# Optimization experiments

Hardware: AMD Instinct MI355X
Metric: run time of the kernel (lower is better)

Reference implementation:

```python
import jax, jax.numpy as jnp
import numpy as np


def _dct2(x):
    """DCT-II over last dim, scipy norm=None scaling (matches the torch rfft trick:
    X_k = 2 * sum_n x_n cos(pi*k*(2n+1)/(2N))). Expressed as one batched matmul."""
    N = x.shape[-1]
    n = jnp.arange(N, dtype=x.dtype)
    k = jnp.arange(N, dtype=x.dtype)
    # D[k, n] = 2*cos(pi*k*(2n+1)/(2N))
    D = 2.0 * jnp.cos((np.pi / (2.0 * N)) * k[:, None] * (2.0 * n[None, :] + 1.0))
    return jnp.einsum('kn,bcn->bck', D, x)


def setup_inputs() -> dict:
    key = jax.random.key(0)
    k0, k1, k2 = jax.random.split(key, 3)
    b, c, l = 32, 512, 1024
    x = jax.random.normal(k0, (b, c, l), dtype=jnp.float32)
    # 1x1 Conv1d weights (kernel_size=1, bias=False) stored as [out, in]
    w1 = jax.random.normal(k1, (2 * c, c), dtype=jnp.float32) / np.float32(np.sqrt(c))
    w2 = jax.random.normal(k2, (c, 2 * c), dtype=jnp.float32) / np.float32(np.sqrt(2 * c))
    ln_w = jnp.ones((l,), dtype=jnp.float32)
    ln_b = jnp.zeros((l,), dtype=jnp.float32)
    return {"x": x, "w1": w1, "w2": w2, "ln_w": ln_w, "ln_b": ln_b}


def reference(x, w1, w2, ln_w, ln_b):
    eps = 1e-6
    freq = _dct2(x)                                   # [b, c, l]
    mu = jnp.mean(freq, axis=-1, keepdims=True)
    var = jnp.var(freq, axis=-1, keepdims=True)       # biased, like nn.LayerNorm
    h = (freq - mu) * jax.lax.rsqrt(var + eps) * ln_w + ln_b
    # fc: Conv1d(c->2c, k=1) -> Dropout(eval: identity) -> ReLU -> Conv1d(2c->c) -> Sigmoid
    h = jax.nn.relu(jnp.einsum('oi,bil->bol', w1, h))  # [b, 2c, l]
    gate = jax.nn.sigmoid(jnp.einsum('oi,bil->bol', w2, h))  # [b, c, l]
    return x * gate
```

## Files before the change

### kernel.cpp

```cpp
#include <hip/hip_runtime.h>
#include <hip/hip_bf16.h>
#include <math.h>

typedef short short8 __attribute__((ext_vector_type(8)));
typedef short short4v __attribute__((ext_vector_type(4)));
typedef float f32x4 __attribute__((ext_vector_type(4)));

__device__ __forceinline__ short f2bf(float f) {
  union { float f; unsigned u; } v; v.f = f;
  unsigned r = v.u + 0x7FFFu + ((v.u >> 16) & 1u);
  return (short)(r >> 16);
}
__device__ __forceinline__ float bf2f(short s) {
  union { unsigned u; float f; } v; v.u = ((unsigned)(unsigned short)s) << 16;
  return v.f;
}

__global__ __launch_bounds__(256) void cast_kernel(const float* __restrict__ in,
                                                   short* __restrict__ out, int n4) {
  int i = blockIdx.x * blockDim.x + threadIdx.x;
  if (i < n4) {
    float4 v = ((const float4*)in)[i];
    short4v o;
    o.x = f2bf(v.x); o.y = f2bf(v.y); o.z = f2bf(v.z); o.w = f2bf(v.w);
    ((short4v*)out)[i] = o;
  }
}

__global__ __launch_bounds__(256) void build_D(short* __restrict__ D) {
  int t = blockIdx.x * 256 + threadIdx.x;
  int k = t >> 10, n = t & 1023;
  const float s = 1.5339807878856412e-03f;
  float arg = (s * (float)k) * (float)(2 * n + 1);
  D[t] = f2bf(2.0f * cosf(arg));
}

__global__ __launch_bounds__(256) void ln_stats(const float2* __restrict__ partial,
                                                float2* __restrict__ musd) {
  int n = blockIdx.x * 256 + threadIdx.x;
  float S = 0.f, Q = 0.f;
#pragma unroll
  for (int r = 0; r < 4; ++r) {
    float2 p = partial[(size_t)r * 16384 + n];
    S += p.x; Q += p.y;
  }
  float mu  = S * (1.f / 1024.f);
  float var = Q * (1.f / 1024.f) - mu * mu;
  float2 o; o.x = mu; o.y = rsqrtf(var + 1e-6f);
  musd[n] = o;
}

__global__ __launch_bounds__(256) void ln_apply(short* __restrict__ freqT,
                                                const float2* __restrict__ musd,
                                                const float* __restrict__ lnw,
                                                const float* __restrict__ lnb) {
  int t = blockIdx.x * 256 + threadIdx.x;
  int c8 = t & 63;
  int k  = (t >> 6) & 1023;
  int b  = t >> 16;
  size_t idx = ((size_t)b << 19) + (size_t)k * 512 + (size_t)c8 * 8;
  short8 v = *(const short8*)&freqT[idx];
  float w  = lnw[k];
  float bb = lnb[k];
  const float2* ms = &musd[b * 512 + c8 * 8];
  short8 o;
#pragma unroll
  for (int j = 0; j < 8; ++j) {
    float f = bf2f(v[j]);
    float2 m = ms[j];
    o[j] = f2bf((f - m.x) * m.y * w + bb);
  }
  *(short8*)&freqT[idx] = o;
}

template<int EPI>
__global__ __launch_bounds__(512, 2) void gemm256(
    const short* __restrict__ A, const short* __restrict__ B,
    void* __restrict__ Cout, const float* __restrict__ X,
    float2* __restrict__ P, int K, int NT, long strideA, long strideB)
{
  __shared__ short As[2][16384];
  __shared__ short Bs[2][16384];
  const int tid = threadIdx.x;
  const int l   = tid & 63;
  const int w   = tid >> 6;
  const int wm  = w >> 2;
  const int wn  = w & 3;
  const int l7  = l & 7;
  const int lr  = l & 15;
  const int lhi = l >> 4;

  const int nwg = gridDim.x, q = nwg >> 3, orig = blockIdx.x;
  const int wgid = (orig & 7) * q + (orig >> 3);
  int bx, by, bz;
  if (EPI == 0)      { bx = wgid & 3; by = wgid >> 2;      bz = 0; }
  else if (EPI == 1) { bx = wgid & 3; by = (wgid >> 2) & 3; bz = wgid >> 4; }
  else               { by = wgid & 3; bx = (wgid >> 2) & 1; bz = wgid >> 3; }

  const long row0 = (long)bx * 256, col0 = (long)by * 256;
  const short* Ab = A + (size_t)bz * strideA + (size_t)row0 * K;
  const short* Bb = B + (size_t)bz * strideB + (size_t)col0 * K;

  const int rowb  = w * 8 + (l >> 3);
  const int colel = (l7 ^ (l >> 3)) * 8;
  const int arow = (wm * 128 + lr) * 64;
  const int brow = (wn * 64  + lr) * 64;
  const int sk0 = ((lhi    ) ^ l7) * 8;
  const int sk1 = ((lhi + 4) ^ l7) * 8;

  f32x4 acc[8][4];
#pragma unroll
  for (int i = 0; i < 8; ++i)
#pragma unroll
    for (int j = 0; j < 4; ++j) acc[i][j] = (f32x4){0.f, 0.f, 0.f, 0.f};

#define STAGE(KT, D) do {                                                    \
    const size_t ko_ = (size_t)(KT) * 64 + colel;                            \
    _Pragma("unroll")                                                        \
    for (int r_ = 0; r_ < 4; ++r_)                                           \
      __builtin_amdgcn_global_load_lds(                                      \
        (const __attribute__((address_space(1))) void*)(Ab + (size_t)(r_*64 + rowb)*K + ko_), \
        (__attribute__((address_space(3))) void*)(&As[D][r_*4096 + w*512 + l*8]), 16, 0, 0);  \
    _Pragma("unroll")                                                        \
    for (int r_ = 0; r_ < 4; ++r_)                                           \
      __builtin_amdgcn_global_load_lds(                                      \
        (const __attribute__((address_space(1))) void*)(Bb + (size_t)(r_*64 + rowb)*K + ko_), \
        (__attribute__((address_space(3))) void*)(&Bs[D][r_*4096 + w*512 + l*8]), 16, 0, 0);  \
  } while (0)

  STAGE(0, 0);
  STAGE(1, 1);

  short8 b0, b1, b2, b3;
  int cur = 0;
  for (int kt = 0; kt < NT; ++kt) {
    if (kt + 1 < NT) { asm volatile("s_waitcnt vmcnt(8)" ::: "memory"); }
    else             { asm volatile("s_waitcnt vmcnt(0)" ::: "memory"); }
    __builtin_amdgcn_sched_barrier(0);
    __builtin_amdgcn_s_barrier();
    const short* Ad = As[cur];
    const short* Bd = Bs[cur];
    short8 a0, a1, a2, a3;

#define MFMA_ROW(MI, AV)                                                       \
    acc[MI][0] = __builtin_amdgcn_mfma_f32_16x16x32_bf16(AV, b0, acc[MI][0], 0, 0, 0); \
    acc[MI][1] = __builtin_amdgcn_mfma_f32_16x16x32_bf16(AV, b1, acc[MI][1], 0, 0, 0); \
    acc[MI][2] = __builtin_amdgcn_mfma_f32_16x16x32_bf16(AV, b2, acc[MI][2], 0, 0, 0); \
    acc[MI][3] = __builtin_amdgcn_mfma_f32_16x16x32_bf16(AV, b3, acc[MI][3], 0, 0, 0);

#define PH(MIBASE, SK, LOADB)                                                \
    a0 = *(const short8*)&Ad[arow + (MIBASE + 0) * 1024 + SK];               \
    a1 = *(const short8*)&Ad[arow + (MIBASE + 1) * 1024 + SK];               \
    a2 = *(const short8*)&Ad[arow + (MIBASE + 2) * 1024 + SK];               \
    a3 = *(const short8*)&Ad[arow + (MIBASE + 3) * 1024 + SK];               \
    if (LOADB) {                                                             \
      b0 = *(const short8*)&Bd[brow + 0 * 1024 + SK];                        \
      b1 = *(const short8*)&Bd[brow + 1 * 1024 + SK];                        \
      b2 = *(const short8*)&Bd[brow + 2 * 1024 + SK];                        \
      b3 = *(const short8*)&Bd[brow + 3 * 1024 + SK];                        \
    }                                                                        \
    __builtin_amdgcn_s_barrier();                                            \
    asm volatile("s_waitcnt lgkmcnt(0)" ::: "memory");                       \
    __builtin_amdgcn_sched_barrier(0);                                       \
    __builtin_amdgcn_s_setprio(1);                                           \
    MFMA_ROW(MIBASE + 0, a0); MFMA_ROW(MIBASE + 1, a1);                      \
    MFMA_ROW(MIBASE + 2, a2); MFMA_ROW(MIBASE + 3, a3);                      \
    __builtin_amdgcn_s_setprio(0);                                           \
    __builtin_amdgcn_sched_barrier(0);                                       \
    __builtin_amdgcn_s_barrier();

    PH(0, sk0, 1)
    PH(4, sk0, 0)
    PH(0, sk1, 1)
    PH(4, sk1, 0)

    if (kt + 2 < NT) STAGE(kt + 2, cur);
    cur ^= 1;
  }

  const int rb = (int)row0 + wm * 128 + lhi * 4;
  const int cb = (int)col0 + wn * 64 + lr;
  float sv[4], qv[4];
#pragma unroll
  for (int ni = 0; ni < 4; ++ni) { sv[ni] = 0.f; qv[ni] = 0.f; }

#pragma unroll
  for (int mi = 0; mi < 8; ++mi) {
#pragma unroll
    for (int ni = 0; ni < 4; ++ni) {
#pragma unroll
      for (int j = 0; j < 4; ++j) {
        int r  = rb + mi * 16 + j;
        int cc = cb + ni * 16;
        float v = acc[mi][ni][j];
        if (EPI == 0) {
          sv[ni] += v; qv[ni] += v * v;
          ((short*)Cout)[((size_t)(cc >> 9) << 19) + (size_t)r * 512 + (cc & 511)] = f2bf(v);
        } else if (EPI == 1) {
          ((short*)Cout)[(size_t)bz * 1048576 + (size_t)r * 1024 + cc] = f2bf(v > 0.f ? v : 0.f);
        } else {
          size_t idx = (size_t)bz * 524288 + (size_t)r * 1024 + cc;
          float g = 1.f / (1.f + __expf(-v));
          ((float*)Cout)[idx] = X[idx] * g;
        }
      }
    }
  }

  if (EPI == 0) {
    __syncthreads();
    float* redS = (float*)&As[0][0];
    float* redQ = redS + 2048;
    const int contrib = wm * 4 + lhi;
#pragma unroll
    for (int ni = 0; ni < 4; ++ni) {
      int ccl = wn * 64 + ni * 16 + lr;
      redS[ccl * 8 + contrib] = sv[ni];
      redQ[ccl * 8 + contrib] = qv[ni];
    }
    __syncthreads();
    if (tid < 256) {
      float S = 0.f, Q = 0.f;
#pragma unroll
      for (int i = 0; i < 8; ++i) { S += redS[tid * 8 + i]; Q += redQ[tid * 8 + i]; }
      float2 o; o.x = S; o.y = Q;
      P[(size_t)bx * 16384 + col0 + tid] = o;
    }
  }
#undef PH
#undef MFMA_ROW
#undef STAGE
}

extern "C" void kernel_launch(void* const* d_in, const int* in_sizes, int n_in,
                              void* d_out, int out_size, void* d_ws, size_t ws_size,
                              hipStream_t stream) {
  const float* x    = (const float*)d_in[0];
  const float* w1   = (const float*)d_in[1];
  const float* w2   = (const float*)d_in[2];
  const float* ln_w = (const float*)d_in[3];
  const float* ln_b = (const float*)d_in[4];
  float* out = (float*)d_out;

  char* ws = (char*)d_ws;
  short* x_bf   = (short*)(ws);
  short* D_bf   = (short*)(ws + 33554432);
  short* w1_bf  = (short*)(ws + 35651584);
  short* w2_bf  = (short*)(ws + 36700160);
  short* freqT  = (short*)(ws + 37748736);
  short* z1t    = (short*)(ws + 71303168);
  float2* part  = (float2*)(ws + 138412032);
  float2* musd  = (float2*)(ws + 139460608);

  cast_kernel<<<dim3(16384), dim3(256), 0, stream>>>(x,  x_bf,  16777216 / 4);
  cast_kernel<<<dim3(512),   dim3(256), 0, stream>>>(w1, w1_bf, 524288 / 4);
  cast_kernel<<<dim3(512),   dim3(256), 0, stream>>>(w2, w2_bf, 524288 / 4);
  build_D<<<dim3(4096), dim3(256), 0, stream>>>(D_bf);

  gemm256<0><<<dim3(256), dim3(512), 0, stream>>>(
      D_bf, x_bf, (void*)freqT, nullptr, part, 1024, 16, 0, 0);

  ln_stats<<<dim3(64), dim3(256), 0, stream>>>(part, musd);

  ln_apply<<<dim3(8192), dim3(256), 0, stream>>>(freqT, musd, ln_w, ln_b);

  gemm256<1><<<dim3(512), dim3(512), 0, stream>>>(
      freqT, w1_bf, (void*)z1t, nullptr, nullptr, 512, 8, 524288, 0);

  gemm256<2><<<dim3(256), dim3(512), 0, stream>>>(
      w2_bf, z1t, (void*)out, x, nullptr, 1024, 16, 0, 1048576);
}
```

Baseline: 193.0 us.

## Halve GEMM N-tile, deepen B pipeline, read bf16 x in gate epilogue

New measurement: 212.7 us. +10.2%, slower.

```diff
diff --git a/kernel.cpp b/kernel.cpp
--- a/kernel.cpp
+++ b/kernel.cpp
@@ -76,11 +76,11 @@
 template<int EPI>
 __global__ __launch_bounds__(512, 2) void gemm256(
     const short* __restrict__ A, const short* __restrict__ B,
-    void* __restrict__ Cout, const float* __restrict__ X,
+    void* __restrict__ Cout, const short* __restrict__ XB,
     float2* __restrict__ P, int K, int NT, long strideA, long strideB)
 {
   __shared__ short As[2][16384];
-  __shared__ short Bs[2][16384];
+  __shared__ short Bs[4][8192];
   const int tid = threadIdx.x;
   const int l   = tid & 63;
   const int w   = tid >> 6;
@@ -93,101 +93,109 @@
   const int nwg = gridDim.x, q = nwg >> 3, orig = blockIdx.x;
   const int wgid = (orig & 7) * q + (orig >> 3);
   int bx, by, bz;
-  if (EPI == 0)      { bx = wgid & 3; by = wgid >> 2;      bz = 0; }
-  else if (EPI == 1) { bx = wgid & 3; by = (wgid >> 2) & 3; bz = wgid >> 4; }
-  else               { by = wgid & 3; bx = (wgid >> 2) & 1; bz = wgid >> 3; }
-
-  const long row0 = (long)bx * 256, col0 = (long)by * 256;
+  if (EPI == 0)      { bx = wgid & 3; by = wgid >> 2;       bz = 0; }
+  else if (EPI == 1) { bx = wgid & 3; by = (wgid >> 2) & 7; bz = wgid >> 5; }
+  else               { bx = wgid & 1; by = (wgid >> 1) & 7; bz = wgid >> 4; }
+
+  const long row0 = (long)bx * 256, col0 = (long)by * 128;
   const short* Ab = A + (size_t)bz * strideA + (size_t)row0 * K;
   const short* Bb = B + (size_t)bz * strideB + (size_t)col0 * K;
 
   const int rowb  = w * 8 + (l >> 3);
   const int colel = (l7 ^ (l >> 3)) * 8;
-  const int arow = (wm * 128 + lr) * 64;
-  const int brow = (wn * 64  + lr) * 64;
+  const int arow  = (wm * 128 + lr) * 64;
+  const int brow0 = (wn * 32 + lr) * 64;
+  const int brow1 = brow0 + 1024;
   const int sk0 = ((lhi    ) ^ l7) * 8;
   const int sk1 = ((lhi + 4) ^ l7) * 8;
 
-  f32x4 acc[8][4];
-#pragma unroll
-  for (int i = 0; i < 8; ++i)
-#pragma unroll
-    for (int j = 0; j < 4; ++j) acc[i][j] = (f32x4){0.f, 0.f, 0.f, 0.f};
-
-#define STAGE(KT, D) do {                                                    \
+  f32x4 acc[8][2];
+#pragma unroll
+  for (int i = 0; i < 8; ++i) { acc[i][0] = (f32x4){0,0,0,0}; acc[i][1] = (f32x4){0,0,0,0}; }
+
+#define GLL(SRC, DST) __builtin_amdgcn_global_load_lds(                      \
+      (const __attribute__((address_space(1))) void*)(SRC),                  \
+      (__attribute__((address_space(3))) void*)(DST), 16, 0, 0)
+
+#define STAGE_A(KT, D) do {                                                  \
     const size_t ko_ = (size_t)(KT) * 64 + colel;                            \
     _Pragma("unroll")                                                        \
     for (int r_ = 0; r_ < 4; ++r_)                                           \
-      __builtin_amdgcn_global_load_lds(                                      \
-        (const __attribute__((address_space(1))) void*)(Ab + (size_t)(r_*64 + rowb)*K + ko_), \
-        (__attribute__((address_space(3))) void*)(&As[D][r_*4096 + w*512 + l*8]), 16, 0, 0);  \
-    _Pragma("unroll")                                                        \
-    for (int r_ = 0; r_ < 4; ++r_)                                           \
-      __builtin_amdgcn_global_load_lds(                                      \
-        (const __attribute__((address_space(1))) void*)(Bb + (size_t)(r_*64 + rowb)*K + ko_), \
-        (__attribute__((address_space(3))) void*)(&Bs[D][r_*4096 + w*512 + l*8]), 16, 0, 0);  \
+      GLL(Ab + (size_t)(r_ * 64 + rowb) * K + ko_,                           \
+          &As[D][r_ * 4096 + w * 512 + l * 8]);                              \
   } while (0)
 
-  STAGE(0, 0);
-  STAGE(1, 1);
-
-  short8 b0, b1, b2, b3;
-  int cur = 0;
-  for (int kt = 0; kt < NT; ++kt) {
-    if (kt + 1 < NT) { asm volatile("s_waitcnt vmcnt(8)" ::: "memory"); }
-    else             { asm volatile("s_waitcnt vmcnt(0)" ::: "memory"); }
-    __builtin_amdgcn_sched_barrier(0);
-    __builtin_amdgcn_s_barrier();
-    const short* Ad = As[cur];
-    const short* Bd = Bs[cur];
-    short8 a0, a1, a2, a3;
-
-#define MFMA_ROW(MI, AV)                                                       \
-    acc[MI][0] = __builtin_amdgcn_mfma_f32_16x16x32_bf16(AV, b0, acc[MI][0], 0, 0, 0); \
-    acc[MI][1] = __builtin_amdgcn_mfma_f32_16x16x32_bf16(AV, b1, acc[MI][1], 0, 0, 0); \
-    acc[MI][2] = __builtin_amdgcn_mfma_f32_16x16x32_bf16(AV, b2, acc[MI][2], 0, 0, 0); \
-    acc[MI][3] = __builtin_amdgcn_mfma_f32_16x16x32_bf16(AV, b3, acc[MI][3], 0, 0, 0);
-
-#define PH(MIBASE, SK, LOADB)                                                \
-    a0 = *(const short8*)&Ad[arow + (MIBASE + 0) * 1024 + SK];               \
-    a1 = *(const short8*)&Ad[arow + (MIBASE + 1) * 1024 + SK];               \
-    a2 = *(const short8*)&Ad[arow + (MIBASE + 2) * 1024 + SK];               \
-    a3 = *(const short8*)&Ad[arow + (MIBASE + 3) * 1024 + SK];               \
-    if (LOADB) {                                                             \
-      b0 = *(const short8*)&Bd[brow + 0 * 1024 + SK];                        \
-      b1 = *(const short8*)&Bd[brow + 1 * 1024 + SK];                        \
-      b2 = *(const short8*)&Bd[brow + 2 * 1024 + SK];                        \
-      b3 = *(const short8*)&Bd[brow + 3 * 1024 + SK];                        \
-    }                                                                        \
+#define STAGE_B_Q(KT, S, R) do {                                             \
+    const size_t ko_ = (size_t)(KT) * 64 + colel;                            \
+    GLL(Bb + (size_t)((R) * 64 + rowb) * K + ko_,                            \
+        &Bs[S][(R) * 4096 + w * 512 + l * 8]);                               \
+  } while (0)
+
+  STAGE_B_Q(0, 0, 0); STAGE_B_Q(0, 0, 1);
+  STAGE_B_Q(1, 1, 0); STAGE_B_Q(1, 1, 1);
+  STAGE_A(0, 0);
+  STAGE_B_Q(2, 2, 0); STAGE_B_Q(2, 2, 1);
+  STAGE_A(1, 1);
+
+#define MFMA(AV, BV, C) __builtin_amdgcn_mfma_f32_16x16x32_bf16(AV, BV, C, 0, 0, 0)
+
+#define PH2(SK, SR)                                                          \
+    a0 = *(const short8*)&Ad[arow + 0 * 1024 + (SK)];                        \
+    a1 = *(const short8*)&Ad[arow + 1 * 1024 + (SK)];                        \
+    a2 = *(const short8*)&Ad[arow + 2 * 1024 + (SK)];                        \
+    a3 = *(const short8*)&Ad[arow + 3 * 1024 + (SK)];                        \
+    a4 = *(const short8*)&Ad[arow + 4 * 1024 + (SK)];                        \
+    a5 = *(const short8*)&Ad[arow + 5 * 1024 + (SK)];                        \
+    a6 = *(const short8*)&Ad[arow + 6 * 1024 + (SK)];                        \
+    a7 = *(const short8*)&Ad[arow + 7 * 1024 + (SK)];                        \
+    b0 = *(const short8*)&Bd[brow0 + (SK)];                                  \
+    b1 = *(const short8*)&Bd[brow1 + (SK)];                                  \
+    if (doB) STAGE_B_Q(kt + 3, sB, SR);                                      \
     __builtin_amdgcn_s_barrier();                                            \
     asm volatile("s_waitcnt lgkmcnt(0)" ::: "memory");                       \
     __builtin_amdgcn_sched_barrier(0);                                       \
     __builtin_amdgcn_s_setprio(1);                                           \
-    MFMA_ROW(MIBASE + 0, a0); MFMA_ROW(MIBASE + 1, a1);                      \
-    MFMA_ROW(MIBASE + 2, a2); MFMA_ROW(MIBASE + 3, a3);                      \
+    acc[0][0] = MFMA(a0, b0, acc[0][0]); acc[0][1] = MFMA(a0, b1, acc[0][1]); \
+    acc[1][0] = MFMA(a1, b0, acc[1][0]); acc[1][1] = MFMA(a1, b1, acc[1][1]); \
+    acc[2][0] = MFMA(a2, b0, acc[2][0]); acc[2][1] = MFMA(a2, b1, acc[2][1]); \
+    acc[3][0] = MFMA(a3, b0, acc[3][0]); acc[3][1] = MFMA(a3, b1, acc[3][1]); \
+    acc[4][0] = MFMA(a4, b0, acc[4][0]); acc[4][1] = MFMA(a4, b1, acc[4][1]); \
+    acc[5][0] = MFMA(a5, b0, acc[5][0]); acc[5][1] = MFMA(a5, b1, acc[5][1]); \
+    acc[6][0] = MFMA(a6, b0, acc[6][0]); acc[6][1] = MFMA(a6, b1, acc[6][1]); \
+    acc[7][0] = MFMA(a7, b0, acc[7][0]); acc[7][1] = MFMA(a7, b1, acc[7][1]); \
     __builtin_amdgcn_s_setprio(0);                                           \
     __builtin_amdgcn_sched_barrier(0);                                       \
     __builtin_amdgcn_s_barrier();
 
-    PH(0, sk0, 1)
-    PH(4, sk0, 0)
-    PH(0, sk1, 1)
-    PH(4, sk1, 0)
-
-    if (kt + 2 < NT) STAGE(kt + 2, cur);
+  int cur = 0;
+  for (int kt = 0; kt < NT; ++kt) {
+    if (kt + 2 < NT)       { asm volatile("s_waitcnt vmcnt(6)" ::: "memory"); }
+    else if (kt + 2 == NT) { asm volatile("s_waitcnt vmcnt(4)" ::: "memory"); }
+    else                   { asm volatile("s_waitcnt vmcnt(0)" ::: "memory"); }
+    __builtin_amdgcn_sched_barrier(0);
+    __builtin_amdgcn_s_barrier();
+    const short* Ad = As[cur];
+    const short* Bd = Bs[kt & 3];
+    const int sB = (kt + 3) & 3;
+    const bool doB = (kt + 3) < NT;
+    short8 a0, a1, a2, a3, a4, a5, a6, a7, b0, b1;
+
+    PH2(sk0, 0)
+    PH2(sk1, 1)
+
+    if (kt + 2 < NT) STAGE_A(kt + 2, cur);
     cur ^= 1;
   }
 
   const int rb = (int)row0 + wm * 128 + lhi * 4;
-  const int cb = (int)col0 + wn * 64 + lr;
-  float sv[4], qv[4];
-#pragma unroll
-  for (int ni = 0; ni < 4; ++ni) { sv[ni] = 0.f; qv[ni] = 0.f; }
+  const int cb = (int)col0 + wn * 32 + lr;
+  float sv[2], qv[2];
+  sv[0] = sv[1] = qv[0] = qv[1] = 0.f;
 
 #pragma unroll
   for (int mi = 0; mi < 8; ++mi) {
 #pragma unroll
-    for (int ni = 0; ni < 4; ++ni) {
+    for (int ni = 0; ni < 2; ++ni) {
 #pragma unroll
       for (int j = 0; j < 4; ++j) {
         int r  = rb + mi * 16 + j;
@@ -201,7 +209,7 @@
         } else {
           size_t idx = (size_t)bz * 524288 + (size_t)r * 1024 + cc;
           float g = 1.f / (1.f + __expf(-v));
-          ((float*)Cout)[idx] = X[idx] * g;
+          ((float*)Cout)[idx] = bf2f(XB[idx]) * g;
         }
       }
     }
@@ -210,16 +218,16 @@
   if (EPI == 0) {
     __syncthreads();
     float* redS = (float*)&As[0][0];
-    float* redQ = redS + 2048;
+    float* redQ = redS + 1024;
     const int contrib = wm * 4 + lhi;
 #pragma unroll
-    for (int ni = 0; ni < 4; ++ni) {
-      int ccl = wn * 64 + ni * 16 + lr;
+    for (int ni = 0; ni < 2; ++ni) {
+      int ccl = wn * 32 + ni * 16 + lr;
       redS[ccl * 8 + contrib] = sv[ni];
       redQ[ccl * 8 + contrib] = qv[ni];
     }
     __syncthreads();
-    if (tid < 256) {
+    if (tid < 128) {
       float S = 0.f, Q = 0.f;
 #pragma unroll
       for (int i = 0; i < 8; ++i) { S += redS[tid * 8 + i]; Q += redQ[tid * 8 + i]; }
@@ -227,9 +235,11 @@
       P[(size_t)bx * 16384 + col0 + tid] = o;
     }
   }
-#undef PH
-#undef MFMA_ROW
-#undef STAGE
+#undef PH2
+#undef MFMA
+#undef STAGE_A
+#undef STAGE_B_Q
+#undef GLL
 }
 
 extern "C" void kernel_launch(void* const* d_in, const int* in_sizes, int n_in,
@@ -257,16 +267,16 @@
   cast_kernel<<<dim3(512),   dim3(256), 0, stream>>>(w2, w2_bf, 524288 / 4);
   build_D<<<dim3(4096), dim3(256), 0, stream>>>(D_bf);
 
-  gemm256<0><<<dim3(256), dim3(512), 0, stream>>>(
+  gemm256<0><<<dim3(512), dim3(512), 0, stream>>>(
       D_bf, x_bf, (void*)freqT, nullptr, part, 1024, 16, 0, 0);
 
   ln_stats<<<dim3(64), dim3(256), 0, stream>>>(part, musd);
 
   ln_apply<<<dim3(8192), dim3(256), 0, stream>>>(freqT, musd, ln_w, ln_b);
 
-  gemm256<1><<<dim3(512), dim3(512), 0, stream>>>(
+  gemm256<1><<<dim3(1024), dim3(512), 0, stream>>>(
       freqT, w1_bf, (void*)z1t, nullptr, nullptr, 512, 8, 524288, 0);
 
-  gemm256<2><<<dim3(256), dim3(512), 0, stream>>>(
-      w2_bf, z1t, (void*)out, x, nullptr, 1024, 16, 0, 1048576);
-}
+  gemm256<2><<<dim3(512), dim3(512), 0, stream>>>(
+      w2_bf, z1t, (void*)out, x_bf, nullptr, 1024, 16, 0, 1048576);
+}
```

## Restructure GEMM main loop for LDS-load/MFMA overlap and read bf16 x in epilogue

Applied to the files above, without the earlier changes.

Result: faster. 166.5 us (-13.7%).

```diff
diff --git a/kernel.cpp b/kernel.cpp
--- a/kernel.cpp
+++ b/kernel.cpp
@@ -76,7 +76,7 @@
 template<int EPI>
 __global__ __launch_bounds__(512, 2) void gemm256(
     const short* __restrict__ A, const short* __restrict__ B,
-    void* __restrict__ Cout, const float* __restrict__ X,
+    void* __restrict__ Cout, const short* __restrict__ XB,
     float2* __restrict__ P, int K, int NT, long strideA, long strideB)
 {
   __shared__ short As[2][16384];
@@ -93,7 +93,7 @@
   const int nwg = gridDim.x, q = nwg >> 3, orig = blockIdx.x;
   const int wgid = (orig & 7) * q + (orig >> 3);
   int bx, by, bz;
-  if (EPI == 0)      { bx = wgid & 3; by = wgid >> 2;      bz = 0; }
+  if (EPI == 0)      { bx = wgid & 3; by = wgid >> 2;       bz = 0; }
   else if (EPI == 1) { bx = wgid & 3; by = (wgid >> 2) & 3; bz = wgid >> 4; }
   else               { by = wgid & 3; bx = (wgid >> 2) & 1; bz = wgid >> 3; }
 
@@ -114,67 +114,106 @@
 #pragma unroll
     for (int j = 0; j < 4; ++j) acc[i][j] = (f32x4){0.f, 0.f, 0.f, 0.f};
 
+#define GLL(SRC, DST) __builtin_amdgcn_global_load_lds(                      \
+      (const __attribute__((address_space(1))) void*)(SRC),                  \
+      (__attribute__((address_space(3))) void*)(DST), 16, 0, 0)
+
 #define STAGE(KT, D) do {                                                    \
     const size_t ko_ = (size_t)(KT) * 64 + colel;                            \
     _Pragma("unroll")                                                        \
     for (int r_ = 0; r_ < 4; ++r_)                                           \
-      __builtin_amdgcn_global_load_lds(                                      \
-        (const __attribute__((address_space(1))) void*)(Ab + (size_t)(r_*64 + rowb)*K + ko_), \
-        (__attribute__((address_space(3))) void*)(&As[D][r_*4096 + w*512 + l*8]), 16, 0, 0);  \
+      GLL(Ab + (size_t)(r_ * 64 + rowb) * K + ko_,                           \
+          &As[D][r_ * 4096 + w * 512 + l * 8]);                              \
     _Pragma("unroll")                                                        \
     for (int r_ = 0; r_ < 4; ++r_)                                           \
-      __builtin_amdgcn_global_load_lds(                                      \
-        (const __attribute__((address_space(1))) void*)(Bb + (size_t)(r_*64 + rowb)*K + ko_), \
-        (__attribute__((address_space(3))) void*)(&Bs[D][r_*4096 + w*512 + l*8]), 16, 0, 0);  \
+      GLL(Bb + (size_t)(r_ * 64 + rowb) * K + ko_,                           \
+          &Bs[D][r_ * 4096 + w * 512 + l * 8]);                              \
   } while (0)
 
   STAGE(0, 0);
   STAGE(1, 1);
 
-  short8 b0, b1, b2, b3;
+#define MFMA(AV, BV, C) __builtin_amdgcn_mfma_f32_16x16x32_bf16(AV, BV, C, 0, 0, 0)
+#define QUAD(M0, V0, V1, V2, V3)                                             \
+    __builtin_amdgcn_s_setprio(1);                                           \
+    acc[M0+0][0] = MFMA(V0, b0, acc[M0+0][0]);                               \
+    acc[M0+0][1] = MFMA(V0, b1, acc[M0+0][1]);                               \
+    acc[M0+0][2] = MFMA(V0, b2, acc[M0+0][2]);                               \
+    acc[M0+0][3] = MFMA(V0, b3, acc[M0+0][3]);                               \
+    acc[M0+1][0] = MFMA(V1, b0, acc[M0+1][0]);                               \
+    acc[M0+1][1] = MFMA(V1, b1, acc[M0+1][1]);                               \
+    acc[M0+1][2] = MFMA(V1, b2, acc[M0+1][2]);                               \
+    acc[M0+1][3] = MFMA(V1, b3, acc[M0+1][3]);                               \
+    acc[M0+2][0] = MFMA(V2, b0, acc[M0+2][0]);                               \
+    acc[M0+2][1] = MFMA(V2, b1, acc[M0+2][1]);                               \
+    acc[M0+2][2] = MFMA(V2, b2, acc[M0+2][2]);                               \
+    acc[M0+2][3] = MFMA(V2, b3, acc[M0+2][3]);                               \
+    acc[M0+3][0] = MFMA(V3, b0, acc[M0+3][0]);                               \
+    acc[M0+3][1] = MFMA(V3, b1, acc[M0+3][1]);                               \
+    acc[M0+3][2] = MFMA(V3, b2, acc[M0+3][2]);                               \
+    acc[M0+3][3] = MFMA(V3, b3, acc[M0+3][3]);                               \
+    __builtin_amdgcn_s_setprio(0);                                           \
+    __builtin_amdgcn_sched_barrier(0);
+
   int cur = 0;
   for (int kt = 0; kt < NT; ++kt) {
-    if (kt + 1 < NT) { asm volatile("s_waitcnt vmcnt(8)" ::: "memory"); }
+    if (kt + 2 < NT) { asm volatile("s_waitcnt vmcnt(8)" ::: "memory"); }
     else             { asm volatile("s_waitcnt vmcnt(0)" ::: "memory"); }
     __builtin_amdgcn_sched_barrier(0);
     __builtin_amdgcn_s_barrier();
     const short* Ad = As[cur];
     const short* Bd = Bs[cur];
-    short8 a0, a1, a2, a3;
-
-#define MFMA_ROW(MI, AV)                                                       \
-    acc[MI][0] = __builtin_amdgcn_mfma_f32_16x16x32_bf16(AV, b0, acc[MI][0], 0, 0, 0); \
-    acc[MI][1] = __builtin_amdgcn_mfma_f32_16x16x32_bf16(AV, b1, acc[MI][1], 0, 0, 0); \
-    acc[MI][2] = __builtin_amdgcn_mfma_f32_16x16x32_bf16(AV, b2, acc[MI][2], 0, 0, 0); \
-    acc[MI][3] = __builtin_amdgcn_mfma_f32_16x16x32_bf16(AV, b3, acc[MI][3], 0, 0, 0);
-
-#define PH(MIBASE, SK, LOADB)                                                \
-    a0 = *(const short8*)&Ad[arow + (MIBASE + 0) * 1024 + SK];               \
-    a1 = *(const short8*)&Ad[arow + (MIBASE + 1) * 1024 + SK];               \
-    a2 = *(const short8*)&Ad[arow + (MIBASE + 2) * 1024 + SK];               \
-    a3 = *(const short8*)&Ad[arow + (MIBASE + 3) * 1024 + SK];               \
-    if (LOADB) {                                                             \
-      b0 = *(const short8*)&Bd[brow + 0 * 1024 + SK];                        \
-      b1 = *(const short8*)&Bd[brow + 1 * 1024 + SK];                        \
-      b2 = *(const short8*)&Bd[brow + 2 * 1024 + SK];                        \
-      b3 = *(const short8*)&Bd[brow + 3 * 1024 + SK];                        \
-    }                                                                        \
-    __builtin_amdgcn_s_barrier();                                            \
-    asm volatile("s_waitcnt lgkmcnt(0)" ::: "memory");                       \
-    __builtin_amdgcn_sched_barrier(0);                                       \
-    __builtin_amdgcn_s_setprio(1);                                           \
-    MFMA_ROW(MIBASE + 0, a0); MFMA_ROW(MIBASE + 1, a1);                      \
-    MFMA_ROW(MIBASE + 2, a2); MFMA_ROW(MIBASE + 3, a3);                      \
-    __builtin_amdgcn_s_setprio(0);                                           \
-    __builtin_amdgcn_sched_barrier(0);                                       \
+    short8 a0, a1, a2, a3, a4, a5, a6, a7;
+    short8 b0, b1, b2, b3;
+
+    a0 = *(const short8*)&Ad[arow + 0 * 1024 + sk0];
+    a1 = *(const short8*)&Ad[arow + 1 * 1024 + sk0];
+    a2 = *(const short8*)&Ad[arow + 2 * 1024 + sk0];
+    a3 = *(const short8*)&Ad[arow + 3 * 1024 + sk0];
+    b0 = *(const short8*)&Bd[brow + 0 * 1024 + sk0];
+    b1 = *(const short8*)&Bd[brow + 1 * 1024 + sk0];
+    b2 = *(const short8*)&Bd[brow + 2 * 1024 + sk0];
+    b3 = *(const short8*)&Bd[brow + 3 * 1024 + sk0];
+    __builtin_amdgcn_sched_barrier(0);
+    a4 = *(const short8*)&Ad[arow + 4 * 1024 + sk0];
+    a5 = *(const short8*)&Ad[arow + 5 * 1024 + sk0];
+    a6 = *(const short8*)&Ad[arow + 6 * 1024 + sk0];
+    a7 = *(const short8*)&Ad[arow + 7 * 1024 + sk0];
+    __builtin_amdgcn_sched_barrier(0);
+    asm volatile("s_waitcnt lgkmcnt(4)" ::: "memory");
+    __builtin_amdgcn_sched_barrier(0);
+    QUAD(0, a0, a1, a2, a3)
+
+    short8 c0, c1, c2, c3, c4, c5, c6, c7, e0, e1, e2, e3;
+    c0 = *(const short8*)&Ad[arow + 0 * 1024 + sk1];
+    c1 = *(const short8*)&Ad[arow + 1 * 1024 + sk1];
+    c2 = *(const short8*)&Ad[arow + 2 * 1024 + sk1];
+    c3 = *(const short8*)&Ad[arow + 3 * 1024 + sk1];
+    e0 = *(const short8*)&Bd[brow + 0 * 1024 + sk1];
+    e1 = *(const short8*)&Bd[brow + 1 * 1024 + sk1];
+    e2 = *(const short8*)&Bd[brow + 2 * 1024 + sk1];
+    e3 = *(const short8*)&Bd[brow + 3 * 1024 + sk1];
+    __builtin_amdgcn_sched_barrier(0);
+    asm volatile("s_waitcnt lgkmcnt(8)" ::: "memory");
+    __builtin_amdgcn_sched_barrier(0);
+    QUAD(4, a4, a5, a6, a7)
+
+    c4 = *(const short8*)&Ad[arow + 4 * 1024 + sk1];
+    c5 = *(const short8*)&Ad[arow + 5 * 1024 + sk1];
+    c6 = *(const short8*)&Ad[arow + 6 * 1024 + sk1];
+    c7 = *(const short8*)&Ad[arow + 7 * 1024 + sk1];
+    __builtin_amdgcn_sched_barrier(0);
+    asm volatile("s_waitcnt lgkmcnt(4)" ::: "memory");
+    __builtin_amdgcn_sched_barrier(0);
+    b0 = e0; b1 = e1; b2 = e2; b3 = e3;
+    QUAD(0, c0, c1, c2, c3)
+
+    asm volatile("s_waitcnt lgkmcnt(0)" ::: "memory");
+    __builtin_amdgcn_sched_barrier(0);
     __builtin_amdgcn_s_barrier();
-
-    PH(0, sk0, 1)
-    PH(4, sk0, 0)
-    PH(0, sk1, 1)
-    PH(4, sk1, 0)
-
     if (kt + 2 < NT) STAGE(kt + 2, cur);
+    __builtin_amdgcn_sched_barrier(0);
+    QUAD(4, c4, c5, c6, c7)
     cur ^= 1;
   }
 
@@ -201,7 +240,7 @@
         } else {
           size_t idx = (size_t)bz * 524288 + (size_t)r * 1024 + cc;
           float g = 1.f / (1.f + __expf(-v));
-          ((float*)Cout)[idx] = X[idx] * g;
+          ((float*)Cout)[idx] = bf2f(XB[idx]) * g;
         }
       }
     }
@@ -227,9 +266,10 @@
       P[(size_t)bx * 16384 + col0 + tid] = o;
     }
   }
-#undef PH
-#undef MFMA_ROW
+#undef QUAD
+#undef MFMA
 #undef STAGE
+#undef GLL
 }
 
 extern "C" void kernel_launch(void* const* d_in, const int* in_sizes, int n_in,
@@ -268,5 +308,5 @@
       freqT, w1_bf, (void*)z1t, nullptr, nullptr, 512, 8, 524288, 0);
 
   gemm256<2><<<dim3(256), dim3(512), 0, stream>>>(
-      w2_bf, z1t, (void*)out, x, nullptr, 1024, 16, 0, 1048576);
-}
+      w2_bf, z1t, (void*)out, x_bf, nullptr, 1024, 16, 0, 1048576);
+}
```

## Interleave half-tile global loads with MFMA phases and read bf16 x in epilogue

Applied to the files above, without the earlier changes.

Result: faster. 169.7 us (-12.1%).

```diff
diff --git a/kernel.cpp b/kernel.cpp
--- a/kernel.cpp
+++ b/kernel.cpp
@@ -76,7 +76,7 @@
 template<int EPI>
 __global__ __launch_bounds__(512, 2) void gemm256(
     const short* __restrict__ A, const short* __restrict__ B,
-    void* __restrict__ Cout, const float* __restrict__ X,
+    void* __restrict__ Cout, const short* __restrict__ XB,
     float2* __restrict__ P, int K, int NT, long strideA, long strideB)
 {
   __shared__ short As[2][16384];
@@ -93,7 +93,7 @@
   const int nwg = gridDim.x, q = nwg >> 3, orig = blockIdx.x;
   const int wgid = (orig & 7) * q + (orig >> 3);
   int bx, by, bz;
-  if (EPI == 0)      { bx = wgid & 3; by = wgid >> 2;      bz = 0; }
+  if (EPI == 0)      { bx = wgid & 3; by = wgid >> 2;       bz = 0; }
   else if (EPI == 1) { bx = wgid & 3; by = (wgid >> 2) & 3; bz = wgid >> 4; }
   else               { by = wgid & 3; bx = (wgid >> 2) & 1; bz = wgid >> 3; }
 
@@ -103,10 +103,10 @@
 
   const int rowb  = w * 8 + (l >> 3);
   const int colel = (l7 ^ (l >> 3)) * 8;
-  const int arow = (wm * 128 + lr) * 64;
-  const int brow = (wn * 64  + lr) * 64;
-  const int sk0 = ((lhi    ) ^ l7) * 8;
-  const int sk1 = ((lhi + 4) ^ l7) * 8;
+  const int abase = (wm * 16 + lr) * 64;
+  const int bbase = (wn * 16 + lr) * 64;
+  const int s0 = ((lhi    ) ^ l7) * 8;
+  const int s1 = ((lhi + 4) ^ l7) * 8;
 
   f32x4 acc[8][4];
 #pragma unroll
@@ -114,72 +114,101 @@
 #pragma unroll
     for (int j = 0; j < 4; ++j) acc[i][j] = (f32x4){0.f, 0.f, 0.f, 0.f};
 
-#define STAGE(KT, D) do {                                                    \
-    const size_t ko_ = (size_t)(KT) * 64 + colel;                            \
-    _Pragma("unroll")                                                        \
-    for (int r_ = 0; r_ < 4; ++r_)                                           \
-      __builtin_amdgcn_global_load_lds(                                      \
-        (const __attribute__((address_space(1))) void*)(Ab + (size_t)(r_*64 + rowb)*K + ko_), \
-        (__attribute__((address_space(3))) void*)(&As[D][r_*4096 + w*512 + l*8]), 16, 0, 0);  \
-    _Pragma("unroll")                                                        \
-    for (int r_ = 0; r_ < 4; ++r_)                                           \
-      __builtin_amdgcn_global_load_lds(                                      \
-        (const __attribute__((address_space(1))) void*)(Bb + (size_t)(r_*64 + rowb)*K + ko_), \
-        (__attribute__((address_space(3))) void*)(&Bs[D][r_*4096 + w*512 + l*8]), 16, 0, 0);  \
+#define GLL(SRC, DST) __builtin_amdgcn_global_load_lds(                      \
+      (const __attribute__((address_space(1))) void*)(SRC),                  \
+      (__attribute__((address_space(3))) void*)(DST), 16, 0, 0)
+
+#define ST_HALF(OPb, OPlds, T, H) do {                                       \
+    const size_t ko_ = (size_t)(T) * 64 + colel;                             \
+    const short* sb_ = (OPb) + (size_t)((H) * 128 + rowb) * K + ko_;         \
+    short* db_ = &OPlds[(T) & 1][(H) * 8192 + w * 512 + l * 8];              \
+    GLL(sb_, db_);                                                           \
+    GLL(sb_ + (size_t)64 * K, db_ + 4096);                                   \
   } while (0)
 
-  STAGE(0, 0);
-  STAGE(1, 1);
-
-  short8 b0, b1, b2, b3;
+#define LD(PTR, OFF) (*(const short8*)&(PTR)[OFF])
+#define MFMA(AV, BV, C) __builtin_amdgcn_mfma_f32_16x16x32_bf16(AV, BV, C, 0, 0, 0)
+#define QUAD16(MIH, A0, A1, A2, A3, B0, B1, B2, B3)                          \
+    __builtin_amdgcn_s_setprio(1);                                           \
+    acc[MIH+0][0]=MFMA(A0,B0,acc[MIH+0][0]); acc[MIH+0][1]=MFMA(A0,B1,acc[MIH+0][1]); \
+    acc[MIH+0][2]=MFMA(A0,B2,acc[MIH+0][2]); acc[MIH+0][3]=MFMA(A0,B3,acc[MIH+0][3]); \
+    acc[MIH+1][0]=MFMA(A1,B0,acc[MIH+1][0]); acc[MIH+1][1]=MFMA(A1,B1,acc[MIH+1][1]); \
+    acc[MIH+1][2]=MFMA(A1,B2,acc[MIH+1][2]); acc[MIH+1][3]=MFMA(A1,B3,acc[MIH+1][3]); \
+    acc[MIH+2][0]=MFMA(A2,B0,acc[MIH+2][0]); acc[MIH+2][1]=MFMA(A2,B1,acc[MIH+2][1]); \
+    acc[MIH+2][2]=MFMA(A2,B2,acc[MIH+2][2]); acc[MIH+2][3]=MFMA(A2,B3,acc[MIH+2][3]); \
+    acc[MIH+3][0]=MFMA(A3,B0,acc[MIH+3][0]); acc[MIH+3][1]=MFMA(A3,B1,acc[MIH+3][1]); \
+    acc[MIH+3][2]=MFMA(A3,B2,acc[MIH+3][2]); acc[MIH+3][3]=MFMA(A3,B3,acc[MIH+3][3]); \
+    __builtin_amdgcn_s_setprio(0);
+
+#define SBAR __builtin_amdgcn_s_barrier()
+#define SCHB __builtin_amdgcn_sched_barrier(0)
+#define LGKM0 asm volatile("s_waitcnt lgkmcnt(0)" ::: "memory")
+
+  ST_HALF(Bb, Bs, 0, 0); ST_HALF(Bb, Bs, 0, 1);
+  ST_HALF(Ab, As, 0, 0); ST_HALF(Ab, As, 0, 1);
+  ST_HALF(Bb, Bs, 1, 0); ST_HALF(Bb, Bs, 1, 1);
+  ST_HALF(Ab, As, 1, 0);
+  asm volatile("s_waitcnt vmcnt(6)" ::: "memory");
+  SBAR;
+
+  short8 b00, b01, b10, b11, b20, b21, b30, b31;
+  short8 a0, a1, a2, a3;
   int cur = 0;
   for (int kt = 0; kt < NT; ++kt) {
-    if (kt + 1 < NT) { asm volatile("s_waitcnt vmcnt(8)" ::: "memory"); }
-    else             { asm volatile("s_waitcnt vmcnt(0)" ::: "memory"); }
-    __builtin_amdgcn_sched_barrier(0);
-    __builtin_amdgcn_s_barrier();
     const short* Ad = As[cur];
     const short* Bd = Bs[cur];
-    short8 a0, a1, a2, a3;
-
-#define MFMA_ROW(MI, AV)                                                       \
-    acc[MI][0] = __builtin_amdgcn_mfma_f32_16x16x32_bf16(AV, b0, acc[MI][0], 0, 0, 0); \
-    acc[MI][1] = __builtin_amdgcn_mfma_f32_16x16x32_bf16(AV, b1, acc[MI][1], 0, 0, 0); \
-    acc[MI][2] = __builtin_amdgcn_mfma_f32_16x16x32_bf16(AV, b2, acc[MI][2], 0, 0, 0); \
-    acc[MI][3] = __builtin_amdgcn_mfma_f32_16x16x32_bf16(AV, b3, acc[MI][3], 0, 0, 0);
-
-#define PH(MIBASE, SK, LOADB)                                                \
-    a0 = *(const short8*)&Ad[arow + (MIBASE + 0) * 1024 + SK];               \
-    a1 = *(const short8*)&Ad[arow + (MIBASE + 1) * 1024 + SK];               \
-    a2 = *(const short8*)&Ad[arow + (MIBASE + 2) * 1024 + SK];               \
-    a3 = *(const short8*)&Ad[arow + (MIBASE + 3) * 1024 + SK];               \
-    if (LOADB) {                                                             \
-      b0 = *(const short8*)&Bd[brow + 0 * 1024 + SK];                        \
-      b1 = *(const short8*)&Bd[brow + 1 * 1024 + SK];                        \
-      b2 = *(const short8*)&Bd[brow + 2 * 1024 + SK];                        \
-      b3 = *(const short8*)&Bd[brow + 3 * 1024 + SK];                        \
-    }                                                                        \
-    __builtin_amdgcn_s_barrier();                                            \
-    asm volatile("s_waitcnt lgkmcnt(0)" ::: "memory");                       \
-    __builtin_amdgcn_sched_barrier(0);                                       \
-    __builtin_amdgcn_s_setprio(1);                                           \
-    MFMA_ROW(MIBASE + 0, a0); MFMA_ROW(MIBASE + 1, a1);                      \
-    MFMA_ROW(MIBASE + 2, a2); MFMA_ROW(MIBASE + 3, a3);                      \
-    __builtin_amdgcn_s_setprio(0);                                           \
-    __builtin_amdgcn_sched_barrier(0);                                       \
-    __builtin_amdgcn_s_barrier();
-
-    PH(0, sk0, 1)
-    PH(4, sk0, 0)
-    PH(0, sk1, 1)
-    PH(4, sk1, 0)
-
-    if (kt + 2 < NT) STAGE(kt + 2, cur);
+
+    a0 = LD(Ad, 0 * 2048 + abase + s0);
+    a1 = LD(Ad, 1 * 2048 + abase + s0);
+    a2 = LD(Ad, 2 * 2048 + abase + s0);
+    a3 = LD(Ad, 3 * 2048 + abase + s0);
+    b00 = LD(Bd, bbase + s0);          b01 = LD(Bd, bbase + s1);
+    b10 = LD(Bd, 4096 + bbase + s0);   b11 = LD(Bd, 4096 + bbase + s1);
+    b20 = LD(Bd, 8192 + bbase + s0);
+    b30 = LD(Bd, 12288 + bbase + s0);
+    if (kt + 1 < NT) ST_HALF(Ab, As, kt + 1, 1);
+    SCHB; SBAR;
+    LGKM0; SCHB;
+    QUAD16(0, a0, a1, a2, a3, b00, b10, b20, b30)
+    SCHB; SBAR;
+
+    a0 = LD(Ad, 8192 + 0 * 2048 + abase + s0);
+    a1 = LD(Ad, 8192 + 1 * 2048 + abase + s0);
+    a2 = LD(Ad, 8192 + 2 * 2048 + abase + s0);
+    a3 = LD(Ad, 8192 + 3 * 2048 + abase + s0);
+    b21 = LD(Bd, 8192 + bbase + s1);
+    b31 = LD(Bd, 12288 + bbase + s1);
+    if (kt + 2 < NT) ST_HALF(Bb, Bs, kt + 2, 0);
+    SCHB; SBAR;
+    LGKM0; SCHB;
+    QUAD16(4, a0, a1, a2, a3, b00, b10, b20, b30)
+    SCHB; SBAR;
+
+    a0 = LD(Ad, 0 * 2048 + abase + s1);
+    a1 = LD(Ad, 1 * 2048 + abase + s1);
+    a2 = LD(Ad, 2 * 2048 + abase + s1);
+    a3 = LD(Ad, 3 * 2048 + abase + s1);
+    if (kt + 2 < NT) ST_HALF(Bb, Bs, kt + 2, 1);
+    SCHB; SBAR;
+    LGKM0; SCHB;
+    QUAD16(0, a0, a1, a2, a3, b01, b11, b21, b31)
+    SCHB; SBAR;
+
+    a0 = LD(Ad, 8192 + 0 * 2048 + abase + s1);
+    a1 = LD(Ad, 8192 + 1 * 2048 + abase + s1);
+    a2 = LD(Ad, 8192 + 2 * 2048 + abase + s1);
+    a3 = LD(Ad, 8192 + 3 * 2048 + abase + s1);
+    if (kt + 2 < NT) ST_HALF(Ab, As, kt + 2, 0);
+    if (kt + 2 < NT)      { asm volatile("s_waitcnt vmcnt(6)" ::: "memory"); }
+    else if (kt + 1 < NT) { asm volatile("s_waitcnt vmcnt(0)" ::: "memory"); }
+    SCHB; SBAR;
+    LGKM0; SCHB;
+    QUAD16(4, a0, a1, a2, a3, b01, b11, b21, b31)
+    SCHB; SBAR;
+
     cur ^= 1;
   }
 
-  const int rb = (int)row0 + wm * 128 + lhi * 4;
-  const int cb = (int)col0 + wn * 64 + lr;
   float sv[4], qv[4];
 #pragma unroll
   for (int ni = 0; ni < 4; ++ni) { sv[ni] = 0.f; qv[ni] = 0.f; }
@@ -190,8 +219,8 @@
     for (int ni = 0; ni < 4; ++ni) {
 #pragma unroll
       for (int j = 0; j < 4; ++j) {
-        int r  = rb + mi * 16 + j;
-        int cc = cb + ni * 16;
+        int r  = (int)row0 + (mi >> 2) * 128 + (mi & 3) * 32 + wm * 16 + lhi * 4 + j;
+        int cc = (int)col0 + (ni >> 1) * 128 + (ni & 1) * 64 + wn * 16 + lr;
         float v = acc[mi][ni][j];
         if (EPI == 0) {
           sv[ni] += v; qv[ni] += v * v;
@@ -201,7 +230,7 @@
         } else {
           size_t idx = (size_t)bz * 524288 + (size_t)r * 1024 + cc;
           float g = 1.f / (1.f + __expf(-v));
-          ((float*)Cout)[idx] = X[idx] * g;
+          ((float*)Cout)[idx] = bf2f(XB[idx]) * g;
         }
       }
     }
@@ -214,7 +243,7 @@
     const int contrib = wm * 4 + lhi;
 #pragma unroll
     for (int ni = 0; ni < 4; ++ni) {
-      int ccl = wn * 64 + ni * 16 + lr;
+      int ccl = (ni >> 1) * 128 + (ni & 1) * 64 + wn * 16 + lr;
       redS[ccl * 8 + contrib] = sv[ni];
       redQ[ccl * 8 + contrib] = qv[ni];
     }
@@ -227,9 +256,14 @@
       P[(size_t)bx * 16384 + col0 + tid] = o;
     }
   }
-#undef PH
-#undef MFMA_ROW
-#undef STAGE
+#undef QUAD16
+#undef MFMA
+#undef LD
+#undef ST_HALF
+#undef GLL
+#undef SBAR
+#undef SCHB
+#undef LGKM0
 }
 
 extern "C" void kernel_launch(void* const* d_in, const int* in_sizes, int n_in,
@@ -268,5 +302,5 @@
       freqT, w1_bf, (void*)z1t, nullptr, nullptr, 512, 8, 524288, 0);
 
   gemm256<2><<<dim3(256), dim3(512), 0, stream>>>(
-      w2_bf, z1t, (void*)out, x, nullptr, 1024, 16, 0, 1048576);
-}
+      w2_bf, z1t, (void*)out, x_bf, nullptr, 1024, 16, 0, 1048576);
+}
```
